# Kernel tuning notes

Hardware: AMD Instinct MI355X
Metric: run time of the kernel (lower is better)

The kernel has to match this reference:

```python
import jax, jax.numpy as jnp
import numpy as np

NUM_HEADS = 12   # top-k = num_heads experts selected per token
SWITCHLOSS = 0.1
ZLOSS = 0.001


def setup_inputs() -> dict:
    key = jax.random.key(0)
    ks = jax.random.split(key, 8)
    B, N, C, E, D = 2, 2048, 768, 24, 64
    w = lambda k, shape: (jax.random.normal(k, shape, jnp.float32) * 0.02)
    return {
        "x": jax.random.normal(ks[0], (B, N, C), jnp.float32),
        "w_gate": w(ks[1], (C, E)),
        "W_in": w(ks[2], (E, C, D)),    # per-expert q projection
        "b_in": jnp.zeros((E, D), jnp.float32),
        "W_out": w(ks[3], (E, D, C)),   # per-expert output projection
        "b_out": jnp.zeros((E, C), jnp.float32),
        "W_kv": w(ks[4], (C, 2 * D)),   # shared single-head K/V
        "b_kv": jnp.zeros((2 * D,), jnp.float32),
    }


def reference(x, w_gate, W_in, b_in, W_out, b_out, W_kv, b_kv):
    B, N, C = x.shape
    E, _, D = W_in.shape
    H = NUM_HEADS
    scale = D ** -0.5

    xf = x.reshape(-1, C)                         # [T, C], T = B*N
    # --- top-k gating (k = num_heads) ---
    logits = xf @ w_gate                          # [T, E]
    probs = jax.nn.softmax(logits, axis=-1)
    top_p, idx = jax.lax.top_k(probs, H)          # [T, H]
    gates = top_p / (top_p.sum(-1, keepdims=True) + 1e-6)
    oh = jax.nn.one_hot(idx, E, dtype=x.dtype)    # [T, H, E]
    comb = oh * gates[..., None]                  # gated dispatch/combine weights

    # --- aux losses (switchloss + zloss; cvloss coeff = 0) ---
    dense_gates = comb.sum(1)                     # [T, E]
    freqs = (dense_gates > 0).astype(x.dtype).sum(0)
    p_sum = probs.sum(0)
    switch = E * jnp.sum((p_sum / p_sum.sum()) * (freqs / freqs.sum()))
    z = jnp.mean(jax.nn.logsumexp(logits, axis=1) ** 2)
    aux_loss = SWITCHLOSS * switch + ZLOSS * z

    # --- MoE map: per-token q via selected experts (no gate multiply) ---
    q_all = jnp.einsum('tc,ecd->ted', xf, W_in) + b_in     # [T, E, D]
    q = jnp.take_along_axis(q_all, idx[..., None], axis=1)  # [T, H, D]
    q = q.reshape(B, N, H, D)

    # --- shared-KV attention (multi-query style) ---
    kv = x @ W_kv + b_kv
    k, v = jnp.split(kv, 2, axis=-1)              # [B, N, D] each
    attn = jnp.einsum('bihd,bjd->bhij', q, k) * scale
    attn = jax.nn.softmax(attn, axis=-1)
    o = jnp.einsum('bhij,bjd->bihd', attn, v).reshape(-1, H, D)  # [T, H, D]

    # --- MoE reduce: gated combine through per-expert output projections ---
    xe = jnp.einsum('the,thd->ted', comb, o)      # [T, E, D] gated dispatch
    out = jnp.einsum('ted,edc->tc', xe, W_out) + jnp.einsum('the,ec->tc', comb, b_out)
    return out.reshape(B, N, C), aux_loss
```

## Files before the change

### kernel.cpp

```cpp
#include <hip/hip_runtime.h>
#include <hip/hip_bf16.h>

#define T_  4096
#define Bb  2
#define Nn  2048
#define Cc  768
#define Ee  24
#define Dd  64
#define Hh  12
#define KR  1568
#define KS  16
#define KC  48
#define NB2 1024
#define SCL 0.18033688f

typedef __attribute__((ext_vector_type(8))) short bf16x8;
typedef __attribute__((ext_vector_type(4))) short bf16x4;
typedef __attribute__((ext_vector_type(4))) float f32x4;

__device__ __forceinline__ unsigned short f2bf(float f) {
  union { float f; unsigned int i; } u; u.f = f;
  unsigned int r = u.i + 0x7FFFu + ((u.i >> 16) & 1u);
  return (unsigned short)(r >> 16);
}
__device__ __forceinline__ float bf2f(unsigned short s) {
  union { unsigned int i; float f; } u; u.i = ((unsigned int)s) << 16; return u.f;
}

__device__ __forceinline__ void gload16(const void* g, void* l) {
  __builtin_amdgcn_global_load_lds(
      (const __attribute__((address_space(1))) void*)g,
      (__attribute__((address_space(3))) void*)l, 16, 0, 0);
}

__global__ __launch_bounds__(256) void convert_all_kernel(
    const float* __restrict__ W_in, const float* __restrict__ W_out,
    const float* __restrict__ b_out, const float* __restrict__ W_kv,
    unsigned short* __restrict__ BqT, unsigned short* __restrict__ BrT,
    unsigned short* __restrict__ BkvT)
{
  __shared__ float ls[64 * 129];
  const int bid = blockIdx.x, tid = threadIdx.x;
  if (bid < 288) {
    const int e = bid / 12, c0 = (bid % 12) * 64;
    #pragma unroll
    for (int i = 0; i < 16; ++i) {
      int L = tid + i * 256, c = L >> 6, d = L & 63;
      ls[c * 65 + d] = W_in[(size_t)e * Cc * Dd + (size_t)(c0 + c) * Dd + d];
    }
    __syncthreads();
    #pragma unroll
    for (int i = 0; i < 16; ++i) {
      int L = tid + i * 256, d = L >> 6, c = L & 63;
      BqT[(size_t)(e * Dd + d) * Cc + c0 + c] = f2bf(ls[c * 65 + d]);
    }
  } else if (bid < 876) {
    const int i2 = bid - 288;
    const int k0 = (i2 / 12) * 32, n0 = (i2 % 12) * 64;
    #pragma unroll
    for (int i = 0; i < 8; ++i) {
      int L = tid + i * 256, k = L >> 6, n = L & 63;
      int kk = k0 + k;
      float v = (kk < 1536) ? W_out[(size_t)kk * Cc + n0 + n]
              : (kk < 1560) ? b_out[(size_t)(kk - 1536) * Cc + n0 + n] : 0.f;
      ls[k * 65 + n] = v;
    }
    __syncthreads();
    #pragma unroll
    for (int i = 0; i < 8; ++i) {
      int L = tid + i * 256, n = L >> 5, k = L & 31;
      BrT[(size_t)(n0 + n) * KR + k0 + k] = f2bf(ls[k * 65 + n]);
    }
  } else {
    const int c0 = (bid - 876) * 64;
    #pragma unroll
    for (int i = 0; i < 32; ++i) {
      int L = tid + i * 256, c = L >> 7, j = L & 127;
      ls[c * 129 + j] = W_kv[(size_t)(c0 + c) * 128 + j];
    }
    __syncthreads();
    #pragma unroll
    for (int i = 0; i < 32; ++i) {
      int L = tid + i * 256, j = L >> 6, c = L & 63;
      BkvT[(size_t)j * Cc + c0 + c] = f2bf(ls[c * 129 + j]);
    }
  }
}

template<int MODE, int BM>
__global__ __launch_bounds__(256) void gemm_bt_kernel(
    const unsigned short* __restrict__ A, const unsigned short* __restrict__ BT,
    const float* __restrict__ bias, const float* __restrict__ bias2,
    void* __restrict__ Cout, void* __restrict__ Cout2, void* __restrict__ Cout3,
    int K, int ldc)
{
  constexpr int MI = BM / 32;
  __shared__ __align__(16) unsigned short As[BM * 32];
  __shared__ __align__(16) unsigned short Bs[128 * 32];
  const int tid = threadIdx.x, w = tid >> 6, lane = tid & 63;
  const int quad = lane >> 4, nl = lane & 15;
  const int m0 = blockIdx.x * BM, n0 = blockIdx.y * 128;
  const int mw = (w & 1) * (BM / 2), nw = (w >> 1) * 64;

  f32x4 acc[MI][4];
  #pragma unroll
  for (int i = 0; i < MI; ++i)
    #pragma unroll
    for (int j = 0; j < 4; ++j) acc[i][j] = (f32x4){0.f, 0.f, 0.f, 0.f};

  const int rlane = lane >> 2, col8 = (lane & 3) * 8;
  const int row0a = w * (BM / 4) + rlane;
  const int row0b = w * 32 + rlane;
  const unsigned short* a0 = A + (size_t)(m0 + row0a) * K + col8;
  const unsigned short* a1 = a0 + (size_t)16 * K;
  const unsigned short* b0 = BT + (size_t)(n0 + row0b) * K + col8;
  const unsigned short* b1 = b0 + (size_t)16 * K;
  unsigned short* lA0 = As + (w * (BM / 4)) * 32;
  unsigned short* lA1 = As + (w * (BM / 4) + 16) * 32;
  unsigned short* lB0 = Bs + (w * 32) * 32;
  unsigned short* lB1 = Bs + (w * 32 + 16) * 32;

  for (int k0 = 0; k0 < K; k0 += 32) {
    gload16(a0 + k0, lA0);
    if (BM == 128) gload16(a1 + k0, lA1);
    gload16(b0 + k0, lB0);
    gload16(b1 + k0, lB1);
    __syncthreads();

    bf16x8 af[MI], bfr[4];
    #pragma unroll
    for (int mi = 0; mi < MI; ++mi)
      af[mi] = *(const bf16x8*)&As[(mw + mi * 16 + nl) * 32 + quad * 8];
    #pragma unroll
    for (int ni = 0; ni < 4; ++ni)
      bfr[ni] = *(const bf16x8*)&Bs[(nw + ni * 16 + nl) * 32 + quad * 8];
    #pragma unroll
    for (int mi = 0; mi < MI; ++mi)
      #pragma unroll
      for (int ni = 0; ni < 4; ++ni)
        acc[mi][ni] = __builtin_amdgcn_mfma_f32_16x16x32_bf16(
            af[mi], bfr[ni], acc[mi][ni], 0, 0, 0);
    __syncthreads();
  }

  #pragma unroll
  for (int mi = 0; mi < MI; ++mi) {
    int rowb = m0 + mw + mi * 16 + quad * 4;
    int bb = rowb >> 11, nn = rowb & (Nn - 1);
    #pragma unroll
    for (int ni = 0; ni < 4; ++ni) {
      int col = n0 + nw + ni * 16 + nl;
      if (MODE == 0) {
        #pragma unroll
        for (int reg = 0; reg < 4; ++reg)
          ((float*)Cout)[(size_t)(rowb + reg) * ldc + col] = acc[mi][ni][reg];
      } else {
        if (col < 1536) {
          float bv = bias[col];
          #pragma unroll
          for (int reg = 0; reg < 4; ++reg)
            ((unsigned short*)Cout)[(size_t)(rowb + reg) * 1536 + col] =
                f2bf((acc[mi][ni][reg] + bv) * SCL);
        } else {
          int c2 = col - 1536;
          float bv = bias2[c2];
          if (c2 < Dd) {
            #pragma unroll
            for (int reg = 0; reg < 4; ++reg)
              ((unsigned short*)Cout2)[((size_t)bb * Nn + nn + reg) * Dd + c2] =
                  f2bf(acc[mi][ni][reg] + bv);
          } else {
            int p6 = nn & 63;
            int np = (nn & ~63) | (p6 & 0x23)
                   | (((p6 >> 4) & 1) << 2) | (((p6 >> 2) & 3) << 3);
            ushort4 v;
            v.x = f2bf(acc[mi][ni][0] + bv);
            v.y = f2bf(acc[mi][ni][1] + bv);
            v.z = f2bf(acc[mi][ni][2] + bv);
            v.w = f2bf(acc[mi][ni][3] + bv);
            *(ushort4*)((unsigned short*)Cout3 +
                        ((size_t)bb * Dd + (c2 - Dd)) * Nn + np) = v;
          }
        }
      }
    }
  }
}

#define XPAD 52
__global__ __launch_bounds__(256) void gate1_kernel(
    const float* __restrict__ x, const float* __restrict__ wg,
    float* __restrict__ partial, unsigned short* __restrict__ xb)
{
  __shared__ __align__(16) float xs[256 * XPAD];
  __shared__ __align__(16) float wsT[Ee * KC];
  const int tid = threadIdx.x;
  const int t0 = blockIdx.x * 256;
  const int s = blockIdx.y, k0 = s * KC;

  #pragma unroll
  for (int i = 0; i < 12; ++i) {
    int f = tid + i * 256;
    int token = f / 12, j = f % 12;
    size_t gofs = (size_t)(t0 + token) * Cc + k0 + j * 4;
    float4 v = *(const float4*)&x[gofs];
    *(float4*)&xs[token * XPAD + j * 4] = v;
    ushort4 o;
    o.x = f2bf(v.x); o.y = f2bf(v.y); o.z = f2bf(v.z); o.w = f2bf(v.w);
    *(ushort4*)&xb[gofs] = o;
  }
  for (int i = tid; i < Ee * KC; i += 256)
    wsT[(i % Ee) * KC + i / Ee] = wg[k0 * Ee + i];
  __syncthreads();

  float xr[KC];
  #pragma unroll
  for (int kg = 0; kg < KC / 4; ++kg)
    *(float4*)&xr[kg * 4] = *(const float4*)&xs[tid * XPAD + kg * 4];

  float acc[Ee];
  #pragma unroll
  for (int e = 0; e < Ee; ++e) acc[e] = 0.f;
  #pragma unroll
  for (int e = 0; e < Ee; ++e) {
    #pragma unroll
    for (int kg = 0; kg < KC / 4; ++kg) {
      float4 wv = *(const float4*)&wsT[e * KC + kg * 4];
      acc[e] += xr[kg * 4 + 0] * wv.x + xr[kg * 4 + 1] * wv.y
              + xr[kg * 4 + 2] * wv.z + xr[kg * 4 + 3] * wv.w;
    }
  }

  float* dst = partial + ((size_t)(t0 + tid) * KS + s) * Ee;
  #pragma unroll
  for (int eg = 0; eg < Ee / 4; ++eg)
    *(float4*)&dst[eg * 4] = *(float4*)&acc[eg * 4];
}

__global__ __launch_bounds__(256) void gate2_kernel(
    const float* __restrict__ partial,
    int* __restrict__ idx, float* __restrict__ gate, float* __restrict__ bstats)
{
  __shared__ float xls[4][KS * Ee];
  __shared__ float sacc[49];
  const int tid = threadIdx.x;
  const int w = tid >> 6, lane = tid & 63;
  const int t = blockIdx.x * 4 + w;

  if (tid < 49) sacc[tid] = 0.f;

  const float* p = partial + (size_t)t * (KS * Ee);
  #pragma unroll
  for (int i = 0; i < 6; ++i) xls[w][lane + i * 64] = p[lane + i * 64];

  float logit = -1e30f;
  if (lane < Ee) {
    float acc = 0.f;
    #pragma unroll
    for (int s = 0; s < KS; ++s) acc += xls[w][s * Ee + lane];
    logit = acc;
  }
  float m = logit;
  for (int o = 32; o; o >>= 1) m = fmaxf(m, __shfl_xor(m, o));
  float pr = (lane < Ee) ? expf(logit - m) : 0.f;
  float s = pr;
  for (int o = 32; o; o >>= 1) s += __shfl_xor(s, o);
  float prob = pr / s;
  float lse = m + logf(s);

  bool sel = false;
  float my_p = 0.f; int my_e = -1;
  for (int h = 0; h < Hh; ++h) {
    float v = (lane < Ee && !sel) ? prob : -1.f;
    int ix = lane;
    for (int o = 32; o; o >>= 1) {
      float ov = __shfl_xor(v, o); int oi = __shfl_xor(ix, o);
      if (ov > v || (ov == v && oi < ix)) { v = ov; ix = oi; }
    }
    if (lane == ix) sel = true;
    if (lane == h) { my_p = v; my_e = ix; }
  }
  float gsum = (lane < Hh) ? my_p : 0.f;
  for (int o = 32; o; o >>= 1) gsum += __shfl_xor(gsum, o);
  if (lane < Hh) {
    idx[t * Hh + lane] = my_e;
    gate[t * Hh + lane] = my_p / (gsum + 1e-6f);
  }

  __syncthreads();
  if (lane < Ee) atomicAdd(&sacc[lane], prob);
  if (lane < Hh) atomicAdd(&sacc[24 + my_e], 1.0f);
  if (lane == 0) atomicAdd(&sacc[48], lse * lse);
  __syncthreads();
  if (tid < 49) bstats[(size_t)tid * NB2 + blockIdx.x] = sacc[tid];
}

__global__ __launch_bounds__(256, 6) void attn_kernel(
    const unsigned short* __restrict__ qallb, const int* __restrict__ idx,
    const unsigned short* __restrict__ kbuf, const unsigned short* __restrict__ vtbuf,
    float* __restrict__ opart, float* __restrict__ lpart)
{
  __shared__ __align__(16) unsigned short ksl[64 * 64];
  __shared__ __align__(16) unsigned short vtl[64 * 64];

  const int tid = threadIdx.x;
  const int w = tid >> 6, lane = tid & 63;
  const int quad = lane >> 4, nl = lane & 15;
  const int bh = blockIdx.y;
  const int b = bh / Hh, h = bh - b * Hh;
  const int qw = blockIdx.x * 64 + w * 16;
  const int sp = blockIdx.z;
  const int jbeg = sp * (Nn / 2);

  const int tq = b * Nn + qw + nl;
  const int eq = idx[tq * Hh + h];
  const unsigned short* qrow = qallb + (size_t)tq * (Ee * Dd) + eq * Dd + quad * 8;
  const bf16x8 qB0 = *(const bf16x8*)(qrow);
  const bf16x8 qB1 = *(const bf16x8*)(qrow + 32);

  f32x4 acc[4];
  #pragma unroll
  for (int dg = 0; dg < 4; ++dg) acc[dg] = (f32x4){0.f, 0.f, 0.f, 0.f};
  float l = 0.f;

  const int sr  = lane >> 3;
  const int cbd = (lane & 7) ^ sr;
  const int xl  = nl & 7;
  const int ca0 = (quad ^ xl) * 8;
  const int ca1 = ((quad + 4) ^ xl) * 8;

  for (int j0 = jbeg; j0 < jbeg + Nn / 2; j0 += 64) {
    #pragma unroll
    for (int i = 0; i < 2; ++i) {
      int r = w * 16 + i * 8;
      gload16(kbuf + ((size_t)b * Nn + j0 + r + sr) * Dd + cbd * 8, ksl + r * 64);
      gload16(vtbuf + ((size_t)b * Dd + r + sr) * Nn + j0 + cbd * 8, vtl + r * 64);
    }
    __syncthreads();

    __builtin_amdgcn_s_setprio(1);
    bf16x4 pf[4];
    #pragma unroll
    for (int kg = 0; kg < 4; ++kg) {
      const unsigned short* kr = ksl + (kg * 16 + nl) * 64;
      bf16x8 a0 = *(const bf16x8*)(kr + ca0);
      bf16x8 a1 = *(const bf16x8*)(kr + ca1);
      f32x4 c = {0.f, 0.f, 0.f, 0.f};
      c = __builtin_amdgcn_mfma_f32_16x16x32_bf16(a0, qB0, c, 0, 0, 0);
      c = __builtin_amdgcn_mfma_f32_16x16x32_bf16(a1, qB1, c, 0, 0, 0);
      float p0 = __builtin_amdgcn_exp2f(c[0]);
      float p1 = __builtin_amdgcn_exp2f(c[1]);
      float p2 = __builtin_amdgcn_exp2f(c[2]);
      float p3 = __builtin_amdgcn_exp2f(c[3]);
      l += (p0 + p1) + (p2 + p3);
      union { __hip_bfloat162 h2[2]; bf16x4 v; } pk;
      pk.h2[0] = __float22bfloat162_rn(float2{p0, p1});
      pk.h2[1] = __float22bfloat162_rn(float2{p2, p3});
      pf[kg] = pk.v;
    }
    bf16x8 pb0 = __builtin_shufflevector(pf[0], pf[1], 0, 1, 2, 3, 4, 5, 6, 7);
    bf16x8 pb1 = __builtin_shufflevector(pf[2], pf[3], 0, 1, 2, 3, 4, 5, 6, 7);
    #pragma unroll
    for (int dg = 0; dg < 4; ++dg) {
      const unsigned short* vrow = vtl + (dg * 16 + nl) * 64;
      bf16x8 v0 = *(const bf16x8*)(vrow + ca0);
      bf16x8 v1 = *(const bf16x8*)(vrow + ca1);
      acc[dg] = __builtin_amdgcn_mfma_f32_16x16x32_bf16(v0, pb0, acc[dg], 0, 0, 0);
      acc[dg] = __builtin_amdgcn_mfma_f32_16x16x32_bf16(v1, pb1, acc[dg], 0, 0, 0);
    }
    __builtin_amdgcn_s_setprio(0);
    __syncthreads();
  }

  float lg = l;
  lg += __shfl_xor(lg, 16);
  lg += __shfl_xor(lg, 32);
  if (lane < 16)
    lpart[(size_t)sp * (Bb * Hh * Nn) + (size_t)bh * Nn + qw + nl] = lg;
  float* orow = opart + (size_t)sp * ((size_t)Bb * Hh * Nn * Dd)
              + ((size_t)bh * Nn + qw + nl) * Dd + quad * 4;
  #pragma unroll
  for (int dg = 0; dg < 4; ++dg) {
    float4 o;
    o.x = acc[dg][0]; o.y = acc[dg][1];
    o.z = acc[dg][2]; o.w = acc[dg][3];
    *(float4*)(orow + dg * 16) = o;
  }
}

__global__ __launch_bounds__(256) void scatter_kernel(
    const float* __restrict__ opart, const float* __restrict__ lpart,
    const int* __restrict__ idx, const float* __restrict__ gate,
    unsigned short* __restrict__ xeg)
{
  __shared__ int   sel[Ee];
  __shared__ float glh[Hh];
  __shared__ float gg[Hh];
  const int t = blockIdx.x, b = t >> 11, nn = t & (Nn - 1);
  const int tid = threadIdx.x;
  const size_t HN = (size_t)Bb * Hh * Nn;
  if (tid < Ee) sel[tid] = -1;
  __syncthreads();
  if (tid < Hh) {
    int e = idx[t * Hh + tid];
    sel[e] = tid;
    float g = gate[t * Hh + tid];
    gg[tid] = g;
    size_t row = (size_t)(b * Hh + tid) * Nn + nn;
    glh[tid] = g / (lpart[row] + lpart[HN + row]);
  }
  __syncthreads();
  for (int c = tid; c < KR; c += 256) {
    float v = 0.f;
    if (c < 1536) {
      int e = c >> 6, h = sel[e];
      if (h >= 0) {
        size_t oofs = ((size_t)(b * Hh + h) * Nn + nn) * Dd + (c & 63);
        v = glh[h] * (opart[oofs] + opart[HN * Dd + oofs]);
      }
    } else if (c < 1560) {
      int h = sel[c - 1536];
      if (h >= 0) v = gg[h];
    }
    xeg[(size_t)t * KR + c] = f2bf(v);
  }
}

__global__ __launch_bounds__(256) void aux1_kernel(
    const float* __restrict__ bstats, float* __restrict__ stats2)
{
  __shared__ float r[4];
  const int j = blockIdx.x, tid = threadIdx.x;
  float4 v = *(const float4*)&bstats[(size_t)j * NB2 + tid * 4];
  float s = (v.x + v.y) + (v.z + v.w);
  for (int o = 32; o; o >>= 1) s += __shfl_xor(s, o);
  if ((tid & 63) == 0) r[tid >> 6] = s;
  __syncthreads();
  if (tid == 0) stats2[j] = (r[0] + r[1]) + (r[2] + r[3]);
}

__global__ void aux2_kernel(const float* __restrict__ stats2,
                            float* __restrict__ out, int out_size)
{
  const int lane = threadIdx.x;
  float a = (lane < Ee) ? stats2[lane] : 0.f;
  float b = (lane < Ee) ? stats2[24 + lane] : 0.f;
  float pt = a, ft = b, sw = a * b;
  for (int o = 32; o; o >>= 1) {
    pt += __shfl_xor(pt, o); ft += __shfl_xor(ft, o); sw += __shfl_xor(sw, o);
  }
  if (lane == 0) {
    float sswitch = (float)Ee * sw / (pt * ft);
    float z = stats2[48] * (1.0f / (float)T_);
    out[out_size - 1] = 0.1f * sswitch + 0.001f * z;
  }
}

extern "C" void kernel_launch(void* const* d_in, const int* in_sizes, int n_in,
                              void* d_out, int out_size, void* d_ws, size_t ws_size,
                              hipStream_t stream)
{
  const float* x     = (const float*)d_in[0];
  const float* wg    = (const float*)d_in[1];
  const float* W_in  = (const float*)d_in[2];
  const float* b_in  = (const float*)d_in[3];
  const float* W_out = (const float*)d_in[4];
  const float* b_out = (const float*)d_in[5];
  const float* W_kv  = (const float*)d_in[6];
  const float* b_kv  = (const float*)d_in[7];
  float* out = (float*)d_out;

  char* ws = (char*)d_ws;
  size_t off = 0;
  auto carve = [&](size_t bytes) -> void* {
    void* p = ws + off;
    off = (off + bytes + 255) & ~(size_t)255;
    return p;
  };
  int*            idx    = (int*)           carve((size_t)T_ * Hh * 4);
  float*          gate   = (float*)         carve((size_t)T_ * Hh * 4);
  float*          bstats = (float*)         carve((size_t)49 * NB2 * 4);
  float*          stats2 = (float*)         carve(256);
  float*          lpart  = (float*)         carve((size_t)2 * Bb * Hh * Nn * 4);
  float*          lgate  = (float*)         carve((size_t)T_ * KS * Ee * 4);
  unsigned short* xb     = (unsigned short*)carve((size_t)T_ * Cc * 2);
  unsigned short* BqkvT  = (unsigned short*)carve((size_t)(Ee * Dd + 128) * Cc * 2);
  unsigned short* BkvT   = BqkvT + (size_t)Ee * Dd * Cc;
  unsigned short* BrT    = (unsigned short*)carve((size_t)Cc * KR * 2);
  unsigned short* kbuf   = (unsigned short*)carve((size_t)T_ * Dd * 2);
  unsigned short* vtbuf  = (unsigned short*)carve((size_t)T_ * Dd * 2);
  unsigned short* qallb  = (unsigned short*)carve((size_t)T_ * Ee * Dd * 2);
  float*          opart  = (float*)         carve((size_t)2 * Bb * Hh * Nn * Dd * 4);
  unsigned short* xeg    = (unsigned short*)carve((size_t)T_ * KR * 2);

  convert_all_kernel<<<888, 256, 0, stream>>>(
      W_in, W_out, b_out, W_kv, BqkvT, BrT, BkvT);

  gate1_kernel<<<dim3(T_ / 256, KS), 256, 0, stream>>>(x, wg, lgate, xb);
  gate2_kernel<<<NB2, 256, 0, stream>>>(lgate, idx, gate, bstats);

  gemm_bt_kernel<1, 64><<<dim3(T_ / 64, 13), 256, 0, stream>>>(
      xb, BqkvT, b_in, b_kv, qallb, kbuf, vtbuf, Cc, 1536);

  attn_kernel<<<dim3(Nn / 64, Bb * Hh, 2), 256, 0, stream>>>(
      qallb, idx, kbuf, vtbuf, opart, lpart);

  scatter_kernel<<<T_, 256, 0, stream>>>(opart, lpart, idx, gate, xeg);

  gemm_bt_kernel<0, 64><<<dim3(T_ / 64, Cc / 128), 256, 0, stream>>>(
      xeg, BrT, nullptr, nullptr, out, nullptr, nullptr, KR, Cc);

  aux1_kernel<<<49, 256, 0, stream>>>(bstats, stats2);
  aux2_kernel<<<1, 64, 0, stream>>>(stats2, out, out_size);
}
```

Baseline: 209.3 us.

## Triple-buffer K/V tiles in attention and drop the two-way key split

The attention kernel now stages K and V^T tiles into a 3-deep LDS ring with explicit vmcnt waits and barriers, so global loads for later tiles overlap MFMA compute on the current one. The key-dimension split across blockIdx.z is removed, so each block walks the full 2048 keys and writes a single partial. The scatter kernel no longer sums two partials, which halves opart/lpart traffic. In exchange the grid is half the size with lower occupancy (launch bound 3) and more LDS per block, and correctness relies on hand-counted vmcnt values.

```diff
diff --git a/kernel.cpp b/kernel.cpp
--- a/kernel.cpp
+++ b/kernel.cpp
@@ -295,13 +295,13 @@
   if (tid < 49) bstats[(size_t)tid * NB2 + blockIdx.x] = sacc[tid];
 }
 
-__global__ __launch_bounds__(256, 6) void attn_kernel(
+__global__ __launch_bounds__(256, 3) void attn_kernel(
     const unsigned short* __restrict__ qallb, const int* __restrict__ idx,
     const unsigned short* __restrict__ kbuf, const unsigned short* __restrict__ vtbuf,
     float* __restrict__ opart, float* __restrict__ lpart)
 {
-  __shared__ __align__(16) unsigned short ksl[64 * 64];
-  __shared__ __align__(16) unsigned short vtl[64 * 64];
+  __shared__ __align__(16) unsigned short ksl[3][64 * 64];
+  __shared__ __align__(16) unsigned short vtl[3][64 * 64];
 
   const int tid = threadIdx.x;
   const int w = tid >> 6, lane = tid & 63;
@@ -309,8 +309,6 @@
   const int bh = blockIdx.y;
   const int b = bh / Hh, h = bh - b * Hh;
   const int qw = blockIdx.x * 64 + w * 16;
-  const int sp = blockIdx.z;
-  const int jbeg = sp * (Nn / 2);
 
   const int tq = b * Nn + qw + nl;
   const int eq = idx[tq * Hh + h];
@@ -329,20 +327,26 @@
   const int ca0 = (quad ^ xl) * 8;
   const int ca1 = ((quad + 4) ^ xl) * 8;
 
-  for (int j0 = jbeg; j0 < jbeg + Nn / 2; j0 += 64) {
+  const unsigned short* kgbase =
+      kbuf + ((size_t)b * Nn + w * 16 + sr) * Dd + cbd * 8;
+  const unsigned short* vgbase =
+      vtbuf + ((size_t)b * Dd + w * 16 + sr) * Nn + cbd * 8;
+
+  auto STAGE = [&](int bi, int t) {
+    const int j0 = t * 64;
     #pragma unroll
     for (int i = 0; i < 2; ++i) {
-      int r = w * 16 + i * 8;
-      gload16(kbuf + ((size_t)b * Nn + j0 + r + sr) * Dd + cbd * 8, ksl + r * 64);
-      gload16(vtbuf + ((size_t)b * Dd + r + sr) * Nn + j0 + cbd * 8, vtl + r * 64);
-    }
-    __syncthreads();
-
+      gload16(kgbase + (size_t)(j0 + i * 8) * Dd, &ksl[bi][(w * 16 + i * 8) * 64]);
+      gload16(vgbase + (size_t)(i * 8) * Nn + j0, &vtl[bi][(w * 16 + i * 8) * 64]);
+    }
+  };
+
+  auto COMPUTE = [&](const unsigned short* ks_, const unsigned short* vt_) {
     __builtin_amdgcn_s_setprio(1);
     bf16x4 pf[4];
     #pragma unroll
     for (int kg = 0; kg < 4; ++kg) {
-      const unsigned short* kr = ksl + (kg * 16 + nl) * 64;
+      const unsigned short* kr = ks_ + (kg * 16 + nl) * 64;
       bf16x8 a0 = *(const bf16x8*)(kr + ca0);
       bf16x8 a1 = *(const bf16x8*)(kr + ca1);
       f32x4 c = {0.f, 0.f, 0.f, 0.f};
@@ -362,23 +366,62 @@
     bf16x8 pb1 = __builtin_shufflevector(pf[2], pf[3], 0, 1, 2, 3, 4, 5, 6, 7);
     #pragma unroll
     for (int dg = 0; dg < 4; ++dg) {
-      const unsigned short* vrow = vtl + (dg * 16 + nl) * 64;
+      const unsigned short* vrow = vt_ + (dg * 16 + nl) * 64;
       bf16x8 v0 = *(const bf16x8*)(vrow + ca0);
       bf16x8 v1 = *(const bf16x8*)(vrow + ca1);
       acc[dg] = __builtin_amdgcn_mfma_f32_16x16x32_bf16(v0, pb0, acc[dg], 0, 0, 0);
       acc[dg] = __builtin_amdgcn_mfma_f32_16x16x32_bf16(v1, pb1, acc[dg], 0, 0, 0);
     }
     __builtin_amdgcn_s_setprio(0);
-    __syncthreads();
-  }
+  };
+
+  STAGE(0, 0);
+  STAGE(1, 1);
+  #pragma unroll 1
+  for (int t = 0; t < 30; t += 3) {
+    STAGE(2, t + 2);
+    asm volatile("s_waitcnt vmcnt(8)" ::: "memory");
+    __builtin_amdgcn_s_barrier();
+    __builtin_amdgcn_sched_barrier(0);
+    COMPUTE(ksl[0], vtl[0]);
+    __builtin_amdgcn_sched_barrier(0);
+    asm volatile("" ::: "memory");
+    __builtin_amdgcn_s_barrier();
+
+    STAGE(0, t + 3);
+    asm volatile("s_waitcnt vmcnt(8)" ::: "memory");
+    __builtin_amdgcn_s_barrier();
+    __builtin_amdgcn_sched_barrier(0);
+    COMPUTE(ksl[1], vtl[1]);
+    __builtin_amdgcn_sched_barrier(0);
+    asm volatile("" ::: "memory");
+    __builtin_amdgcn_s_barrier();
+
+    STAGE(1, t + 4);
+    asm volatile("s_waitcnt vmcnt(8)" ::: "memory");
+    __builtin_amdgcn_s_barrier();
+    __builtin_amdgcn_sched_barrier(0);
+    COMPUTE(ksl[2], vtl[2]);
+    __builtin_amdgcn_sched_barrier(0);
+    asm volatile("" ::: "memory");
+    __builtin_amdgcn_s_barrier();
+  }
+  asm volatile("s_waitcnt vmcnt(4)" ::: "memory");
+  __builtin_amdgcn_s_barrier();
+  __builtin_amdgcn_sched_barrier(0);
+  COMPUTE(ksl[0], vtl[0]);
+  __builtin_amdgcn_sched_barrier(0);
+  asm volatile("s_waitcnt vmcnt(0)" ::: "memory");
+  __builtin_amdgcn_s_barrier();
+  __builtin_amdgcn_sched_barrier(0);
+  COMPUTE(ksl[1], vtl[1]);
 
   float lg = l;
   lg += __shfl_xor(lg, 16);
   lg += __shfl_xor(lg, 32);
   if (lane < 16)
-    lpart[(size_t)sp * (Bb * Hh * Nn) + (size_t)bh * Nn + qw + nl] = lg;
-  float* orow = opart + (size_t)sp * ((size_t)Bb * Hh * Nn * Dd)
-              + ((size_t)bh * Nn + qw + nl) * Dd + quad * 4;
+    lpart[(size_t)bh * Nn + qw + nl] = lg;
+  float* orow = opart + ((size_t)bh * Nn + qw + nl) * Dd + quad * 4;
   #pragma unroll
   for (int dg = 0; dg < 4; ++dg) {
     float4 o;
@@ -398,7 +441,6 @@
   __shared__ float gg[Hh];
   const int t = blockIdx.x, b = t >> 11, nn = t & (Nn - 1);
   const int tid = threadIdx.x;
-  const size_t HN = (size_t)Bb * Hh * Nn;
   if (tid < Ee) sel[tid] = -1;
   __syncthreads();
   if (tid < Hh) {
@@ -407,7 +449,7 @@
     float g = gate[t * Hh + tid];
     gg[tid] = g;
     size_t row = (size_t)(b * Hh + tid) * Nn + nn;
-    glh[tid] = g / (lpart[row] + lpart[HN + row]);
+    glh[tid] = g / lpart[row];
   }
   __syncthreads();
   for (int c = tid; c < KR; c += 256) {
@@ -416,7 +458,7 @@
       int e = c >> 6, h = sel[e];
       if (h >= 0) {
         size_t oofs = ((size_t)(b * Hh + h) * Nn + nn) * Dd + (c & 63);
-        v = glh[h] * (opart[oofs] + opart[HN * Dd + oofs]);
+        v = glh[h] * opart[oofs];
       }
     } else if (c < 1560) {
       int h = sel[c - 1536];
@@ -481,7 +523,7 @@
   float*          gate   = (float*)         carve((size_t)T_ * Hh * 4);
   float*          bstats = (float*)         carve((size_t)49 * NB2 * 4);
   float*          stats2 = (float*)         carve(256);
-  float*          lpart  = (float*)         carve((size_t)2 * Bb * Hh * Nn * 4);
+  float*          lpart  = (float*)         carve((size_t)Bb * Hh * Nn * 4);
   float*          lgate  = (float*)         carve((size_t)T_ * KS * Ee * 4);
   unsigned short* xb     = (unsigned short*)carve((size_t)T_ * Cc * 2);
   unsigned short* BqkvT  = (unsigned short*)carve((size_t)(Ee * Dd + 128) * Cc * 2);
@@ -490,7 +532,7 @@
   unsigned short* kbuf   = (unsigned short*)carve((size_t)T_ * Dd * 2);
   unsigned short* vtbuf  = (unsigned short*)carve((size_t)T_ * Dd * 2);
   unsigned short* qallb  = (unsigned short*)carve((size_t)T_ * Ee * Dd * 2);
-  float*          opart  = (float*)         carve((size_t)2 * Bb * Hh * Nn * Dd * 4);
+  float*          opart  = (float*)         carve((size_t)Bb * Hh * Nn * Dd * 4);
   unsigned short* xeg    = (unsigned short*)carve((size_t)T_ * KR * 2);
 
   convert_all_kernel<<<888, 256, 0, stream>>>(
@@ -502,7 +544,7 @@
   gemm_bt_kernel<1, 64><<<dim3(T_ / 64, 13), 256, 0, stream>>>(
       xb, BqkvT, b_in, b_kv, qallb, kbuf, vtbuf, Cc, 1536);
 
-  attn_kernel<<<dim3(Nn / 64, Bb * Hh, 2), 256, 0, stream>>>(
+  attn_kernel<<<dim3(Nn / 64, Bb * Hh), 256, 0, stream>>>(
       qallb, idx, kbuf, vtbuf, opart, lpart);
 
   scatter_kernel<<<T_, 256, 0, stream>>>(opart, lpart, idx, gate, xeg);
```

Result: no change. 207.1 us (-1.0%).
